# Kernel tuning notes

Measured on AMD Instinct MI355X. Metric: run time of the kernel, lower is better.

## Reference

```python
import jax, jax.numpy as jnp
import numpy as np

T = 524288
D = 256
N = 8192

def setup_inputs() -> dict:
    key = jax.random.key(0)
    k1, k2, k3 = jax.random.split(key, 3)
    embedding = jax.random.normal(k1, (T, D), dtype=jnp.float32)
    W = jax.random.normal(k2, (D, D), dtype=jnp.float32) * (1.0 / np.sqrt(D))
    obj_to_img = jnp.sort(jax.random.randint(k3, (T,), 0, N))
    return {"embedding": embedding, "W": W, "obj_to_img": obj_to_img, "num_segments": N}

def reference(embedding, W, obj_to_img, num_segments):
    # Per-segment mean of embedding @ W  -> global context [N, D]
    proj = embedding @ W  # [T, D]
    seg_sum = jax.ops.segment_sum(proj, obj_to_img, num_segments=num_segments)  # [N, D]
    counts = jax.ops.segment_sum(jnp.ones((embedding.shape[0],), embedding.dtype),
                                 obj_to_img, num_segments=num_segments)  # [N]
    safe_counts = jnp.maximum(counts, 1.0)
    transformed_global = jnp.tanh(seg_sum / safe_counts[:, None])  # [N, D]
    # sigmoid(emb . tg[segment]) per token
    scores = jax.nn.sigmoid(jnp.sum(embedding * transformed_global[obj_to_img], axis=-1))  # [T]
    # per-segment weighted sum of embeddings
    rep = jax.ops.segment_sum(embedding * scores[:, None], obj_to_img, num_segments=num_segments)  # [N, D]
    # broadcast representation back to every token of its segment (repeat_interleave)
    return rep[obj_to_img]  # [T, D]
```

## Files before the change

### kernel.cpp

```cpp
#include <hip/hip_runtime.h>
#include <math.h>

#define D 256
#define NSEG 8192

typedef float f4_t __attribute__((ext_vector_type(4)));

__global__ __launch_bounds__(256) void seg_starts_kernel(
        const int* __restrict__ obj, int T, int* __restrict__ starts) {
    const int i = blockIdx.x * blockDim.x + threadIdx.x;
    if (i >= T) return;
    const int cur  = obj[i];
    const int prev = (i == 0) ? -1 : obj[i - 1];
    for (int s = prev + 1; s <= cur; ++s) starts[s] = i;
    if (i == T - 1) {
        for (int s = cur + 1; s <= NSEG; ++s) starts[s] = T;
    }
}

__device__ __forceinline__ int lower_bound_dev(const int* __restrict__ a, int n, int key) {
    int lo = 0, hi = n;
    while (lo < hi) {
        int mid = (lo + hi) >> 1;
        if (a[mid] < key) lo = mid + 1; else hi = mid;
    }
    return lo;
}

__device__ __forceinline__ float dot4(const float4 a, const float4 b) {
    return a.x * b.x + a.y * b.y + a.z * b.z + a.w * b.w;
}

__device__ __forceinline__ float4 ld4(const float* p) {
    return *reinterpret_cast<const float4*>(p);
}

template <bool USE_STARTS>
__global__ __launch_bounds__(256) void fused_seg_kernel(
        const float* __restrict__ emb,
        const float* __restrict__ W,
        const int*   __restrict__ obj, int T,
        const int*   __restrict__ starts,
        float* __restrict__ out) {
    const int seg = blockIdx.x;
    int start, end;
    if (USE_STARTS) {
        start = starts[seg];
        end   = starts[seg + 1];
    } else {
        start = lower_bound_dev(obj, T, seg);
        end   = lower_bound_dev(obj, T, seg + 1);
    }
    if (start >= end) return;

    const int tid  = threadIdx.x;
    const int lane = tid & 63;
    const int w    = tid >> 6;
    const int col  = lane * 4;

    __shared__ float sm[4][D];
    __shared__ float sv[D];
    __shared__ float tg[D];

    const float* ebase = emb + col;

    float4 acc = make_float4(0.f, 0.f, 0.f, 0.f);
    {
        int r = start + w;
        for (; r + 12 < end; r += 16) {
            const float4 e0 = ld4(ebase + (size_t)r * D);
            const float4 e1 = ld4(ebase + (size_t)(r + 4) * D);
            const float4 e2 = ld4(ebase + (size_t)(r + 8) * D);
            const float4 e3 = ld4(ebase + (size_t)(r + 12) * D);
            acc.x += (e0.x + e1.x) + (e2.x + e3.x);
            acc.y += (e0.y + e1.y) + (e2.y + e3.y);
            acc.z += (e0.z + e1.z) + (e2.z + e3.z);
            acc.w += (e0.w + e1.w) + (e2.w + e3.w);
        }
        for (; r < end; r += 4) {
            const float4 e0 = ld4(ebase + (size_t)r * D);
            acc.x += e0.x; acc.y += e0.y; acc.z += e0.z; acc.w += e0.w;
        }
    }
    *reinterpret_cast<float4*>(&sm[w][col]) = acc;
    __syncthreads();
    sv[tid] = sm[0][tid] + sm[1][tid] + sm[2][tid] + sm[3][tid];
    __syncthreads();

    const float inv = 1.0f / (float)(end - start);
    float4 p4 = make_float4(0.f, 0.f, 0.f, 0.f);
    {
        const float* Wp = W + (size_t)(64 * w) * D + col;
        const float* svp = &sv[64 * w];
        #pragma unroll 8
        for (int kk = 0; kk < 64; ++kk) {
            const float  s  = svp[kk];
            const float4 wr = ld4(Wp + (size_t)kk * D);
            p4.x += s * wr.x; p4.y += s * wr.y;
            p4.z += s * wr.z; p4.w += s * wr.w;
        }
    }
    *reinterpret_cast<float4*>(&sm[w][col]) = p4;
    __syncthreads();
    const float pj = sm[0][tid] + sm[1][tid] + sm[2][tid] + sm[3][tid];
    tg[tid] = tanhf(pj * inv);
    __syncthreads();
    const float4 tg4 = ld4(&tg[col]);

    float4 racc = make_float4(0.f, 0.f, 0.f, 0.f);
    {
        int r = start + w;
        for (; r + 12 < end; r += 16) {
            const float4 e0 = ld4(ebase + (size_t)r * D);
            const float4 e1 = ld4(ebase + (size_t)(r + 4) * D);
            const float4 e2 = ld4(ebase + (size_t)(r + 8) * D);
            const float4 e3 = ld4(ebase + (size_t)(r + 12) * D);
            float pd0 = dot4(e0, tg4);
            float pd1 = dot4(e1, tg4);
            float pd2 = dot4(e2, tg4);
            float pd3 = dot4(e3, tg4);
            #pragma unroll
            for (int off = 32; off >= 1; off >>= 1) {
                pd0 += __shfl_xor(pd0, off, 64);
                pd1 += __shfl_xor(pd1, off, 64);
                pd2 += __shfl_xor(pd2, off, 64);
                pd3 += __shfl_xor(pd3, off, 64);
            }
            const float s0 = 1.0f / (1.0f + __expf(-pd0));
            const float s1 = 1.0f / (1.0f + __expf(-pd1));
            const float s2 = 1.0f / (1.0f + __expf(-pd2));
            const float s3 = 1.0f / (1.0f + __expf(-pd3));
            racc.x += (e0.x * s0 + e1.x * s1) + (e2.x * s2 + e3.x * s3);
            racc.y += (e0.y * s0 + e1.y * s1) + (e2.y * s2 + e3.y * s3);
            racc.z += (e0.z * s0 + e1.z * s1) + (e2.z * s2 + e3.z * s3);
            racc.w += (e0.w * s0 + e1.w * s1) + (e2.w * s2 + e3.w * s3);
        }
        for (; r < end; r += 4) {
            const float4 e0 = ld4(ebase + (size_t)r * D);
            float pd0 = dot4(e0, tg4);
            #pragma unroll
            for (int off = 32; off >= 1; off >>= 1) pd0 += __shfl_xor(pd0, off, 64);
            const float s0 = 1.0f / (1.0f + __expf(-pd0));
            racc.x += e0.x * s0; racc.y += e0.y * s0;
            racc.z += e0.z * s0; racc.w += e0.w * s0;
        }
    }
    *reinterpret_cast<float4*>(&sm[w][col]) = racc;
    __syncthreads();
    sm[0][tid] = sm[0][tid] + sm[1][tid] + sm[2][tid] + sm[3][tid];
    __syncthreads();
    const float4 rep4 = ld4(&sm[0][col]);
    const f4_t repv = { rep4.x, rep4.y, rep4.z, rep4.w };

    {
        float* obase = out + col;
        int r = start + w;
        for (; r + 12 < end; r += 16) {
            __builtin_nontemporal_store(repv, reinterpret_cast<f4_t*>(obase + (size_t)r * D));
            __builtin_nontemporal_store(repv, reinterpret_cast<f4_t*>(obase + (size_t)(r + 4) * D));
            __builtin_nontemporal_store(repv, reinterpret_cast<f4_t*>(obase + (size_t)(r + 8) * D));
            __builtin_nontemporal_store(repv, reinterpret_cast<f4_t*>(obase + (size_t)(r + 12) * D));
        }
        for (; r < end; r += 4) {
            __builtin_nontemporal_store(repv, reinterpret_cast<f4_t*>(obase + (size_t)r * D));
        }
    }
}

extern "C" void kernel_launch(void* const* d_in, const int* in_sizes, int n_in,
                              void* d_out, int out_size, void* d_ws, size_t ws_size,
                              hipStream_t stream) {
    const float* emb = (const float*)d_in[0];
    const float* W   = (const float*)d_in[1];
    const int*   obj = (const int*)d_in[2];
    const int T = in_sizes[2];
    float* out = (float*)d_out;

    if (d_ws != nullptr && ws_size >= (size_t)(NSEG + 1) * sizeof(int)) {
        int* starts = (int*)d_ws;
        seg_starts_kernel<<<(T + 255) / 256, 256, 0, stream>>>(obj, T, starts);
        fused_seg_kernel<true><<<NSEG, 256, 0, stream>>>(emb, W, obj, T, starts, out);
    } else {
        fused_seg_kernel<false><<<NSEG, 256, 0, stream>>>(emb, W, obj, T, nullptr, out);
    }
}
```

Measured before the change: 909.6 us.

## Cache segment embedding rows in registers to avoid re-reading them in the score pass

Each wave now loads up to 20 of its segment rows into a register array once and reuses them for both the mean accumulation and the sigmoid-weighted sum. Segments average 64 rows, so most fit within the 80-row cache. This removes the second global or L2 read of the embeddings. It raises register pressure (80 VGPRs for the cache) and sets launch_bounds to 4 blocks per CU to keep occupancy. It also unrolls the W projection loop further.

```diff
diff --git a/kernel.cpp b/kernel.cpp
--- a/kernel.cpp
+++ b/kernel.cpp
@@ -3,6 +3,7 @@
 
 #define D 256
 #define NSEG 8192
+#define RROWS 20
 
 typedef float f4_t __attribute__((ext_vector_type(4)));
 
@@ -36,7 +37,7 @@
 }
 
 template <bool USE_STARTS>
-__global__ __launch_bounds__(256) void fused_seg_kernel(
+__global__ __launch_bounds__(256, 4) void fused_seg_kernel(
         const float* __restrict__ emb,
         const float* __restrict__ W,
         const int*   __restrict__ obj, int T,
@@ -63,24 +64,24 @@
     __shared__ float tg[D];
 
     const float* ebase = emb + col;
+    const int rbase = start + w;
 
+    float4 cache[RROWS];
+    #pragma unroll
+    for (int i = 0; i < RROWS; ++i) {
+        const int r = rbase + 4 * i;
+        cache[i] = (r < end) ? ld4(ebase + (size_t)r * D)
+                             : make_float4(0.f, 0.f, 0.f, 0.f);
+    }
     float4 acc = make_float4(0.f, 0.f, 0.f, 0.f);
-    {
-        int r = start + w;
-        for (; r + 12 < end; r += 16) {
-            const float4 e0 = ld4(ebase + (size_t)r * D);
-            const float4 e1 = ld4(ebase + (size_t)(r + 4) * D);
-            const float4 e2 = ld4(ebase + (size_t)(r + 8) * D);
-            const float4 e3 = ld4(ebase + (size_t)(r + 12) * D);
-            acc.x += (e0.x + e1.x) + (e2.x + e3.x);
-            acc.y += (e0.y + e1.y) + (e2.y + e3.y);
-            acc.z += (e0.z + e1.z) + (e2.z + e3.z);
-            acc.w += (e0.w + e1.w) + (e2.w + e3.w);
-        }
-        for (; r < end; r += 4) {
-            const float4 e0 = ld4(ebase + (size_t)r * D);
-            acc.x += e0.x; acc.y += e0.y; acc.z += e0.z; acc.w += e0.w;
-        }
+    #pragma unroll
+    for (int i = 0; i < RROWS; ++i) {
+        acc.x += cache[i].x; acc.y += cache[i].y;
+        acc.z += cache[i].z; acc.w += cache[i].w;
+    }
+    for (int r = rbase + 4 * RROWS; r < end; r += 4) {
+        const float4 e = ld4(ebase + (size_t)r * D);
+        acc.x += e.x; acc.y += e.y; acc.z += e.z; acc.w += e.w;
     }
     *reinterpret_cast<float4*>(&sm[w][col]) = acc;
     __syncthreads();
@@ -92,7 +93,7 @@
     {
         const float* Wp = W + (size_t)(64 * w) * D + col;
         const float* svp = &sv[64 * w];
-        #pragma unroll 8
+        #pragma unroll 16
         for (int kk = 0; kk < 64; ++kk) {
             const float  s  = svp[kk];
             const float4 wr = ld4(Wp + (size_t)kk * D);
@@ -108,42 +109,23 @@
     const float4 tg4 = ld4(&tg[col]);
 
     float4 racc = make_float4(0.f, 0.f, 0.f, 0.f);
-    {
-        int r = start + w;
-        for (; r + 12 < end; r += 16) {
-            const float4 e0 = ld4(ebase + (size_t)r * D);
-            const float4 e1 = ld4(ebase + (size_t)(r + 4) * D);
-            const float4 e2 = ld4(ebase + (size_t)(r + 8) * D);
-            const float4 e3 = ld4(ebase + (size_t)(r + 12) * D);
-            float pd0 = dot4(e0, tg4);
-            float pd1 = dot4(e1, tg4);
-            float pd2 = dot4(e2, tg4);
-            float pd3 = dot4(e3, tg4);
-            #pragma unroll
-            for (int off = 32; off >= 1; off >>= 1) {
-                pd0 += __shfl_xor(pd0, off, 64);
-                pd1 += __shfl_xor(pd1, off, 64);
-                pd2 += __shfl_xor(pd2, off, 64);
-                pd3 += __shfl_xor(pd3, off, 64);
-            }
-            const float s0 = 1.0f / (1.0f + __expf(-pd0));
-            const float s1 = 1.0f / (1.0f + __expf(-pd1));
-            const float s2 = 1.0f / (1.0f + __expf(-pd2));
-            const float s3 = 1.0f / (1.0f + __expf(-pd3));
-            racc.x += (e0.x * s0 + e1.x * s1) + (e2.x * s2 + e3.x * s3);
-            racc.y += (e0.y * s0 + e1.y * s1) + (e2.y * s2 + e3.y * s3);
-            racc.z += (e0.z * s0 + e1.z * s1) + (e2.z * s2 + e3.z * s3);
-            racc.w += (e0.w * s0 + e1.w * s1) + (e2.w * s2 + e3.w * s3);
-        }
-        for (; r < end; r += 4) {
-            const float4 e0 = ld4(ebase + (size_t)r * D);
-            float pd0 = dot4(e0, tg4);
-            #pragma unroll
-            for (int off = 32; off >= 1; off >>= 1) pd0 += __shfl_xor(pd0, off, 64);
-            const float s0 = 1.0f / (1.0f + __expf(-pd0));
-            racc.x += e0.x * s0; racc.y += e0.y * s0;
-            racc.z += e0.z * s0; racc.w += e0.w * s0;
-        }
+    #pragma unroll
+    for (int i = 0; i < RROWS; ++i) {
+        float pd = dot4(cache[i], tg4);
+        #pragma unroll
+        for (int off = 32; off >= 1; off >>= 1) pd += __shfl_xor(pd, off, 64);
+        const float s = 1.0f / (1.0f + __expf(-pd));
+        racc.x += cache[i].x * s; racc.y += cache[i].y * s;
+        racc.z += cache[i].z * s; racc.w += cache[i].w * s;
+    }
+    for (int r = rbase + 4 * RROWS; r < end; r += 4) {
+        const float4 e = ld4(ebase + (size_t)r * D);
+        float pd = dot4(e, tg4);
+        #pragma unroll
+        for (int off = 32; off >= 1; off >>= 1) pd += __shfl_xor(pd, off, 64);
+        const float s = 1.0f / (1.0f + __expf(-pd));
+        racc.x += e.x * s; racc.y += e.y * s;
+        racc.z += e.z * s; racc.w += e.w * s;
     }
     *reinterpret_cast<float4*>(&sm[w][col]) = racc;
     __syncthreads();
@@ -154,7 +136,7 @@
 
     {
         float* obase = out + col;
-        int r = start + w;
+        int r = rbase;
         for (; r + 12 < end; r += 16) {
             __builtin_nontemporal_store(repv, reinterpret_cast<f4_t*>(obase + (size_t)r * D));
             __builtin_nontemporal_store(repv, reinterpret_cast<f4_t*>(obase + (size_t)(r + 4) * D));
```

After: 973.9 us. 7.1% more time.
